# Optimization experiments

Hardware: AMD Instinct MI355X
Metric: run time of the kernel (lower is better)

## Reference

```python
import jax, jax.numpy as jnp
import numpy as np

B, G, N = 32, 512, 512          # batch, group (POMO rollouts), problem size
EMB, H, DK = 128, 8, 16          # embedding_dim, head_num, qkv_dim (H*DK == EMB)
E, FH, K = 8, 512, 2             # num_experts, ff_hidden_dim, top-k
SQRT_EMB = 11.313708498984761    # sqrt(128), model_params['sqrt_embedding_dim']
CLIP = 10.0                      # logit_clipping


def setup_inputs() -> dict:
    key = jax.random.key(0)
    ks = jax.random.split(key, 22)
    s = 0.05
    d = {}
    d["pref"] = jax.random.uniform(ks[0], (2,), dtype=jnp.float32)
    d["graph"] = jax.random.normal(ks[1], (B, 1, EMB), dtype=jnp.float32)
    d["capacity"] = jax.random.uniform(ks[2], (B, G), dtype=jnp.float32)
    d["encoded_nodes"] = jax.random.normal(ks[3], (B, N, EMB), dtype=jnp.float32)
    d["ninf_mask"] = jnp.zeros((B, G, N), dtype=jnp.float32)
    # hyper-network MLP (note: original has NO activations between hyper_fc layers)
    d["fc1_w"] = jax.random.normal(ks[4], (256, 2)) * s
    d["fc1_b"] = jax.random.normal(ks[5], (256,)) * s
    d["fc2_w"] = jax.random.normal(ks[6], (256, 256)) * s
    d["fc2_b"] = jax.random.normal(ks[7], (256,)) * s
    d["fc3_w"] = jax.random.normal(ks[8], (8, 256)) * s
    d["fc3_b"] = jax.random.normal(ks[9], (8,)) * s
    # hyper heads producing the attention weight matrices (Linear(embd_dim=2, out), no bias)
    d["hWq"] = jax.random.normal(ks[10], ((1 + EMB) * H * DK, 2)) * 0.02
    d["hWk"] = jax.random.normal(ks[11], (EMB * H * DK, 2)) * 0.02
    d["hWv"] = jax.random.normal(ks[12], (EMB * H * DK, 2)) * 0.02
    d["hWc"] = jax.random.normal(ks[13], (EMB * H * DK, 2)) * 0.02
    # MoE combine layer: gating (token input + 8-dim pref embedding) and E expert MLPs
    d["gate_w"] = jax.random.normal(ks[14], (H * DK, E)) * s
    d["gate_pref_w"] = jax.random.normal(ks[15], (8, E)) * s
    d["e_w1"] = jax.random.normal(ks[16], (E, FH, H * DK)) * (1.0 / np.sqrt(H * DK))
    d["e_b1"] = jnp.zeros((E, FH), dtype=jnp.float32)
    d["e_w2"] = jax.random.normal(ks[17], (E, EMB, FH)) * (1.0 / np.sqrt(FH))
    d["e_b2"] = jnp.zeros((E, EMB), dtype=jnp.float32)
    d = {k2: v.astype(jnp.float32) for k2, v in d.items()}
    return d


def _heads(x):  # [B, n, H*DK] -> [B, H, n, DK]
    b, n, _ = x.shape
    return x.reshape(b, n, H, DK).transpose(0, 2, 1, 3)


def reference(pref, graph, capacity, encoded_nodes, ninf_mask,
              fc1_w, fc1_b, fc2_w, fc2_b, fc3_w, fc3_b,
              hWq, hWk, hWv, hWc,
              gate_w, gate_pref_w, e_w1, e_b1, e_w2, e_b2):
    # ---- assign(pref): hypernet generates attention weight matrices ----
    h = fc1_w @ pref + fc1_b
    h = fc2_w @ h + fc2_b
    mid = fc3_w @ h + fc3_b                      # [8] == mid_embd_pref
    Wq = (hWq @ mid[0:2]).reshape(H * DK, 1 + EMB)
    Wk = (hWk @ mid[2:4]).reshape(H * DK, EMB)
    Wv = (hWv @ mid[4:6]).reshape(H * DK, EMB)
    Wc = (hWc @ mid[6:8]).reshape(H * DK, EMB)
    # ---- set_kv ----
    k = _heads(encoded_nodes @ Wk.T)             # [B,H,N,DK]
    v = _heads(encoded_nodes @ Wv.T)
    # ---- forward ----
    inp = jnp.concatenate(
        [jnp.broadcast_to(graph, (B, G, EMB)), capacity[:, :, None]], axis=2)
    q = _heads(inp @ Wq.T)                       # [B,H,G,DK]
    score = jnp.einsum('bhgd,bhnd->bhgn', q, k) / jnp.sqrt(jnp.float32(DK))
    score = score + ninf_mask[:, None, :, :]
    attn = jax.nn.softmax(score, axis=3)
    out = jnp.einsum('bhgn,bhnd->bhgd', attn, v)
    out = out.transpose(0, 2, 1, 3).reshape(B, G, H * DK)   # [B,G,128]
    # ---- MoE combine (noisy top-k gating, deterministic at inference) ----
    logits = out @ gate_w + mid @ gate_pref_w    # [B,G,E]
    vals, idx = jax.lax.top_k(logits, K)
    gv = jax.nn.softmax(vals, axis=-1)           # softmax over selected k (T=1)
    gates = jnp.sum(jax.nn.one_hot(idx, E, dtype=out.dtype) * gv[..., None], axis=-2)
    hdn = jax.nn.relu(jnp.einsum('bgi,ehi->bgeh', out, e_w1) + e_b1)
    y = jnp.einsum('bgeh,eoh->bgeo', hdn, e_w2) + e_b2
    moe_out = jnp.einsum('bgeo,bge->bgo', y, gates)          # [B,G,EMB]
    # ---- combine + tanh-clipped masked softmax over nodes ----
    mh = moe_out @ Wc.T                           # [B,G,EMB]
    sc = jnp.einsum('bge,bne->bgn', mh, encoded_nodes) / SQRT_EMB
    probs = jax.nn.softmax(CLIP * jnp.tanh(sc) + ninf_mask, axis=2)
    return probs
```

## Files before the change

kernel.cpp:

```cpp
#include <hip/hip_runtime.h>


typedef __attribute__((ext_vector_type(8))) __bf16 bf16x8;
typedef __attribute__((ext_vector_type(4))) float f32x4;

static constexpr long OFF_MID   = 0;
static constexpr long OFF_PREFL = 8;
static constexpr long OFF_WL    = 16;
static constexpr long OFF_WKB   = 256;
static constexpr long OFF_WVB   = 8448;
static constexpr long OFF_WCB   = 16640;
static constexpr long OFF_QB    = 24832;
static constexpr long OFF_MFLAG = 28928;
static constexpr long OFF_CNT   = 33024;
static constexpr long OFF_TOK   = 33032;
static constexpr long OFF_WGT   = 164104;
static constexpr long OFF_AO    = 295176;
static constexpr long OFF_Y0    = 1343752;
static constexpr long OFF_Y1    = 2392328;
static constexpr long OFF_ENCB  = 3440904;

__device__ __forceinline__ unsigned f2bf(float x) {
  union { float f; unsigned u; } v; v.f = x;
  return ((v.u + 0x7FFFu + ((v.u >> 16) & 1u)) >> 16) & 0xFFFFu;
}
__device__ __forceinline__ float bflo(unsigned u) {
  union { unsigned u; float f; } v; v.u = u << 16; return v.f;
}
__device__ __forceinline__ float bfhi(unsigned u) {
  union { unsigned u; float f; } v; v.u = u & 0xFFFF0000u; return v.f;
}

__global__ __launch_bounds__(256)
void k_prep1(const float* __restrict__ pref, const float* __restrict__ fc1w,
             const float* __restrict__ fc1b, const float* __restrict__ fc2w,
             const float* __restrict__ fc2b, const float* __restrict__ fc3w,
             const float* __restrict__ fc3b, const float* __restrict__ gpw,
             const float* __restrict__ hWq, const float* __restrict__ mask,
             const float* __restrict__ ew1, const float* __restrict__ ew2,
             const float* __restrict__ enc,
             unsigned short* __restrict__ w1b, unsigned short* __restrict__ w2b,
             unsigned short* __restrict__ encb, float* __restrict__ ws) {
  const int bid = blockIdx.x;
  const int tid = threadIdx.x;
  if (bid == 0) {
    __shared__ float h1[256];
    __shared__ float h2[256];
    __shared__ float mid[8];
    const float p0 = pref[0], p1 = pref[1];
    h1[tid] = fc1w[2*tid]*p0 + fc1w[2*tid+1]*p1 + fc1b[tid];
    __syncthreads();
    float s = 0.f;
    for (int j = 0; j < 256; ++j) s = fmaf(fc2w[tid*256+j], h1[j], s);
    h2[tid] = s + fc2b[tid];
    __syncthreads();
    if (tid < 8) {
      float s2 = 0.f;
      for (int j = 0; j < 256; ++j) s2 = fmaf(fc3w[tid*256+j], h2[j], s2);
      mid[tid] = s2 + fc3b[tid];
    }
    __syncthreads();
    if (tid < 8) {
      ws[OFF_MID + tid] = mid[tid];
      float s3 = 0.f;
      for (int i = 0; i < 8; ++i) s3 = fmaf(mid[i], gpw[i*8 + tid], s3);
      ws[OFF_PREFL + tid] = s3;
      ((int*)(ws + OFF_CNT))[tid] = 0;
    }
    if (tid >= 16 && tid < 144) {
      const int o = tid - 16;
      ws[OFF_WL + o] = hWq[((long)o*129 + 128)*2]*mid[0]
                     + hWq[((long)o*129 + 128)*2 + 1]*mid[1];
    }
    return;
  }
  if (bid <= 3072) {
    const int i = (bid-1)*256 + tid;
    const float* src;
    unsigned short* dst;
    if (i < 131072)      { src = ew1 + (long)i*4;          dst = w1b + (long)i*4; }
    else if (i < 262144) { src = ew2 + (long)(i-131072)*4; dst = w2b + (long)(i-131072)*4; }
    else                 { src = enc + (long)(i-262144)*4; dst = encb + (long)(i-262144)*4; }
    const float4 v = *(const float4*)src;
    uint2 p;
    p.x = f2bf(v.x) | (f2bf(v.y) << 16);
    p.y = f2bf(v.z) | (f2bf(v.w) << 16);
    *(uint2*)dst = p;
    return;
  }
  __shared__ int fl[8];
  const int rowbase = (bid - 3073) * 8;
  const int r = tid >> 5, seg = tid & 31;
  if (tid < 8) fl[tid] = 0;
  __syncthreads();
  const float* mrow = mask + (long)(rowbase + r)*512 + seg*16;
  int nz = 0;
#pragma unroll
  for (int c = 0; c < 4; ++c) {
    const float4 v = *(const float4*)(mrow + c*4);
    nz |= (v.x != 0.f) | (v.y != 0.f) | (v.z != 0.f) | (v.w != 0.f);
  }
  if (nz) atomicOr(&fl[r], 1);
  __syncthreads();
  if (tid < 8) ((char*)(ws + OFF_MFLAG))[rowbase + tid] = (char)fl[tid];
}

__global__ __launch_bounds__(256)
void k_prep2(const float* __restrict__ graph,
             const float* __restrict__ hWq, const float* __restrict__ hWk,
             const float* __restrict__ hWv, const float* __restrict__ hWc,
             float* __restrict__ ws) {
  const int bid = blockIdx.x;
  const int tid = threadIdx.x;
  __shared__ float mid[8];
  __shared__ float g[2][128];
  if (tid < 8) mid[tid] = ws[OFF_MID + tid];
  __syncthreads();
  if (bid < 192) {
    const int i = bid*256 + tid;
    if (i < 16384) {
      ((unsigned short*)(ws + OFF_WKB))[i] =
          (unsigned short)f2bf(hWk[2*i]*mid[2] + hWk[2*i+1]*mid[3]);
    } else if (i < 32768) {
      const int j = i - 16384;
      ((unsigned short*)(ws + OFF_WVB))[j] =
          (unsigned short)f2bf(hWv[2*j]*mid[4] + hWv[2*j+1]*mid[5]);
    } else {
      const int j = i - 32768;
      ((unsigned short*)(ws + OFF_WCB))[j] =
          (unsigned short)f2bf(hWc[2*j]*mid[6] + hWc[2*j+1]*mid[7]);
    }
    return;
  }
  const int qb = bid - 192;
  const int b0 = qb*2;
  {
    const int bb = tid >> 7, ii = tid & 127;
    g[bb][ii] = graph[(b0+bb)*128 + ii];
  }
  __syncthreads();
  const float m0 = mid[0], m1 = mid[1];
  const int bb = tid >> 7, o = tid & 127;
  const float* hq = hWq + (long)o*129*2;
  float acc = 0.f;
  for (int i2 = 0; i2 < 128; ++i2) {
    const float w = hq[2*i2]*m0 + hq[2*i2+1]*m1;
    acc = fmaf(g[bb][i2], w, acc);
  }
  ws[OFF_QB + (b0+bb)*128 + o] = acc;
}

__device__ __forceinline__ bf16x8 ld_frag(const unsigned short* base, int row, int bytecol) {
  const int addr = row*256 + (bytecol ^ ((row & 7) << 4));
  return *(const bf16x8*)((const char*)base + addr);
}

__global__ __launch_bounds__(256)
void k_kv(const unsigned short* __restrict__ encb,
          const unsigned short* __restrict__ wkb,
          const unsigned short* __restrict__ wvb,
          unsigned short* __restrict__ Kb, unsigned short* __restrict__ Vtg) {
  __shared__ unsigned short Ws[128*128];
  __shared__ unsigned short Xs[64*128];
  const int tid = threadIdx.x;
  const int nbase = blockIdx.x * 64;
  const unsigned short* Wb = blockIdx.y ? wvb : wkb;
#pragma unroll
  for (int s = 0; s < 8; ++s) {
    const int id = tid + s*256;
    const int fr = id >> 4, c16 = id & 15;
    const uint4 v = *(const uint4*)(Wb + (long)fr*128 + c16*8);
    *(uint4*)((char*)Ws + fr*256 + ((c16*16) ^ ((fr & 7) << 4))) = v;
  }
#pragma unroll
  for (int s = 0; s < 4; ++s) {
    const int id = tid + s*256;
    const int r = id >> 4, c16 = id & 15;
    const uint4 v = *(const uint4*)(encb + (long)(nbase + r)*128 + c16*8);
    *(uint4*)((char*)Xs + r*256 + ((c16*16) ^ ((r & 7) << 4))) = v;
  }
  __syncthreads();
  const int w = tid >> 6, l = tid & 63, lq = l >> 4, lr = l & 15;
  f32x4 acc[2][4];
#pragma unroll
  for (int a = 0; a < 2; ++a)
#pragma unroll
    for (int m = 0; m < 4; ++m) acc[a][m] = (f32x4){0.f, 0.f, 0.f, 0.f};
#pragma unroll
  for (int ks = 0; ks < 4; ++ks) {
    const int bcol = ks*64 + lq*16;
    const bf16x8 a0 = ld_frag(Ws, (2*w  )*16 + lr, bcol);
    const bf16x8 a1 = ld_frag(Ws, (2*w+1)*16 + lr, bcol);
    const bf16x8 b0 = ld_frag(Xs, 0*16 + lr, bcol);
    const bf16x8 b1 = ld_frag(Xs, 1*16 + lr, bcol);
    const bf16x8 b2 = ld_frag(Xs, 2*16 + lr, bcol);
    const bf16x8 b3 = ld_frag(Xs, 3*16 + lr, bcol);
    acc[0][0] = __builtin_amdgcn_mfma_f32_16x16x32_bf16(a0, b0, acc[0][0], 0, 0, 0);
    acc[0][1] = __builtin_amdgcn_mfma_f32_16x16x32_bf16(a0, b1, acc[0][1], 0, 0, 0);
    acc[0][2] = __builtin_amdgcn_mfma_f32_16x16x32_bf16(a0, b2, acc[0][2], 0, 0, 0);
    acc[0][3] = __builtin_amdgcn_mfma_f32_16x16x32_bf16(a0, b3, acc[0][3], 0, 0, 0);
    acc[1][0] = __builtin_amdgcn_mfma_f32_16x16x32_bf16(a1, b0, acc[1][0], 0, 0, 0);
    acc[1][1] = __builtin_amdgcn_mfma_f32_16x16x32_bf16(a1, b1, acc[1][1], 0, 0, 0);
    acc[1][2] = __builtin_amdgcn_mfma_f32_16x16x32_bf16(a1, b2, acc[1][2], 0, 0, 0);
    acc[1][3] = __builtin_amdgcn_mfma_f32_16x16x32_bf16(a1, b3, acc[1][3], 0, 0, 0);
  }
  if (blockIdx.y == 0) {
#pragma unroll
    for (int obi = 0; obi < 2; ++obi) {
      const int o0 = (2*w + obi)*16 + lq*4;
#pragma unroll
      for (int mb = 0; mb < 4; ++mb) {
        const long n = nbase + mb*16 + lr;
        uint2 pp;
        pp.x = f2bf(acc[obi][mb][0]) | (f2bf(acc[obi][mb][1]) << 16);
        pp.y = f2bf(acc[obi][mb][2]) | (f2bf(acc[obi][mb][3]) << 16);
        *(uint2*)(Kb + n*128 + o0) = pp;
      }
    }
  } else {
    const int b = nbase >> 9;
    const int nn0 = nbase & 511;
#pragma unroll
    for (int obi = 0; obi < 2; ++obi) {
      const int o0 = (2*w + obi)*16 + lq*4;
#pragma unroll
      for (int mb = 0; mb < 4; ++mb) {
        const int nn = nn0 + mb*16 + lr;
#pragma unroll
        for (int j = 0; j < 4; ++j) {
          const int o = o0 + j;
          Vtg[(((long)b*8 + (o >> 4))*16 + (o & 15))*512 + nn] =
              (unsigned short)f2bf(acc[obi][mb][j]);
        }
      }
    }
  }
}

__global__ __launch_bounds__(512, 8)
void k_attn(const unsigned short* __restrict__ Kb,
            const unsigned short* __restrict__ Vtg,
            const float* __restrict__ ws, const float* __restrict__ cap,
            const float* __restrict__ mask, unsigned short* __restrict__ AOb) {
  const int bid = blockIdx.x;
  const int b = bid & 31, h = (bid >> 5) & 7, qh = bid >> 8;
  __shared__ unsigned short Kbf[512*24];
  __shared__ unsigned short Vt[16*536];
  __shared__ unsigned short Ps[8*16*40];
  const int tid = threadIdx.x;
#pragma unroll
  for (int it = 0; it < 2; ++it) {
    const int i = tid + it*512;
    const int n = i >> 1, hf = i & 1;
    const uint4 kv = *(const uint4*)(Kb + (long)(b*512 + n)*128 + h*16 + hf*8);
    *(uint4*)(Kbf + n*24 + hf*8) = kv;
    const int d = i >> 6, c = i & 63;
    const uint4 vv = *(const uint4*)(Vtg + ((long)(b*8 + h)*16 + d)*512 + c*8);
    *(uint4*)(Vt + d*536 + c*8) = vv;
  }
  const int w = tid >> 6, l = tid & 63;
  const int lq = l >> 4, lr = l & 15;
  const int grow = qh*128 + w*16 + lr;
  bf16x8 qf;
  {
    union { uint4 u; bf16x8 v; } cv;
    cv.u = make_uint4(0u, 0u, 0u, 0u);
    if (lq < 2) {
      const float* qbp = ws + OFF_QB + b*128 + h*16 + lq*8;
      const float* wlp = ws + OFF_WL + h*16 + lq*8;
      const float cp = cap[b*512 + grow];
      float qv[8];
#pragma unroll
      for (int j = 0; j < 8; ++j) qv[j] = (qbp[j] + cp*wlp[j]) * 0.25f;
      cv.u.x = f2bf(qv[0]) | (f2bf(qv[1]) << 16);
      cv.u.y = f2bf(qv[2]) | (f2bf(qv[3]) << 16);
      cv.u.z = f2bf(qv[4]) | (f2bf(qv[5]) << 16);
      cv.u.w = f2bf(qv[6]) | (f2bf(qv[7]) << 16);
    }
    qf = cv.v;
  }
  const int mf = ((const char*)(ws + OFF_MFLAG))[b*512 + grow];
  const bool usemask = __any(mf != 0);
  unsigned short* Pw = Ps + w*16*40;
  const int psw = (lr & 3) << 3;
  __syncthreads();
  float lsum = 0.f;
  f32x4 oaccA = {0.f, 0.f, 0.f, 0.f};
  f32x4 oaccB = {0.f, 0.f, 0.f, 0.f};
  const float* mrow = mask + ((long)(b*512 + grow))*512 + lq*4;
#pragma unroll 2
  for (int qc = 0; qc < 16; ++qc) {
    const int n0 = qc*32;
    f32x4 s[2];
#pragma unroll
    for (int nb = 0; nb < 2; ++nb) {
      bf16x8 kf;
      {
        union { uint4 u; bf16x8 v; } cv;
        cv.u = make_uint4(0u, 0u, 0u, 0u);
        if (lq < 2) cv.u = *(const uint4*)(Kbf + (n0 + nb*16 + lr)*24 + lq*8);
        kf = cv.v;
      }
      s[nb] = __builtin_amdgcn_mfma_f32_16x16x32_bf16(
          kf, qf, (f32x4){0.f, 0.f, 0.f, 0.f}, 0, 0, 0);
      if (usemask) {
        const float4 mk = *(const float4*)(mrow + n0 + nb*16);
        s[nb][0] += mk.x; s[nb][1] += mk.y; s[nb][2] += mk.z; s[nb][3] += mk.w;
      }
    }
#pragma unroll
    for (int nb = 0; nb < 2; ++nb) {
      const float e0 = __expf(s[nb][0]);
      const float e1 = __expf(s[nb][1]);
      const float e2 = __expf(s[nb][2]);
      const float e3 = __expf(s[nb][3]);
      lsum += (e0 + e1) + (e2 + e3);
      uint2 pp;
      asm("v_cvt_pk_bf16_f32 %0, %1, %2" : "=v"(pp.x) : "v"(e0), "v"(e1));
      asm("v_cvt_pk_bf16_f32 %0, %1, %2" : "=v"(pp.y) : "v"(e2), "v"(e3));
      *(uint2*)(Pw + lr*40 + ((nb*16 + lq*4) ^ psw)) = pp;
    }
    const bf16x8 va = *(const bf16x8*)(Vt + lr*536 + n0 + lq*8);
    const bf16x8 pb = *(const bf16x8*)(Pw + lr*40 + (lq*8 ^ psw));
    if (qc & 1) oaccB = __builtin_amdgcn_mfma_f32_16x16x32_bf16(va, pb, oaccB, 0, 0, 0);
    else        oaccA = __builtin_amdgcn_mfma_f32_16x16x32_bf16(va, pb, oaccA, 0, 0, 0);
  }
  lsum += __shfl_xor(lsum, 16);
  lsum += __shfl_xor(lsum, 32);
  const float inv = 1.f / lsum;
  uint2 op;
  op.x = f2bf((oaccA[0]+oaccB[0])*inv) | (f2bf((oaccA[1]+oaccB[1])*inv) << 16);
  op.y = f2bf((oaccA[2]+oaccB[2])*inv) | (f2bf((oaccA[3]+oaccB[3])*inv) << 16);
  *(uint2*)(AOb + (long)(b*512 + grow)*128 + h*16 + lq*4) = op;
}

__global__ __launch_bounds__(256)
void k_gate(const unsigned short* __restrict__ AOb, const float* __restrict__ gw,
            float* __restrict__ ws) {
  const int tid = threadIdx.x;
  const int t = blockIdx.x*256 + tid;
  const unsigned short* x = AOb + (long)t*128;
  float lg[8];
  {
    const float* pl = ws + OFF_PREFL;
#pragma unroll
    for (int e = 0; e < 8; ++e) lg[e] = pl[e];
  }
  for (int i = 0; i < 128; i += 8) {
    const uint4 xv = *(const uint4*)(x + i);
    float xf[8];
    xf[0] = bflo(xv.x); xf[1] = bfhi(xv.x);
    xf[2] = bflo(xv.y); xf[3] = bfhi(xv.y);
    xf[4] = bflo(xv.z); xf[5] = bfhi(xv.z);
    xf[6] = bflo(xv.w); xf[7] = bfhi(xv.w);
#pragma unroll
    for (int u = 0; u < 8; ++u) {
      const float xi = xf[u];
      const float4 ga = *(const float4*)(gw + (i+u)*8);
      const float4 gb = *(const float4*)(gw + (i+u)*8 + 4);
      lg[0] = fmaf(xi, ga.x, lg[0]); lg[1] = fmaf(xi, ga.y, lg[1]);
      lg[2] = fmaf(xi, ga.z, lg[2]); lg[3] = fmaf(xi, ga.w, lg[3]);
      lg[4] = fmaf(xi, gb.x, lg[4]); lg[5] = fmaf(xi, gb.y, lg[5]);
      lg[6] = fmaf(xi, gb.z, lg[6]); lg[7] = fmaf(xi, gb.w, lg[7]);
    }
  }
  int i0 = 0; float v0 = lg[0];
#pragma unroll
  for (int e = 1; e < 8; ++e) if (lg[e] > v0) { v0 = lg[e]; i0 = e; }
  int i1 = -1; float v1 = -1e30f;
#pragma unroll
  for (int e = 0; e < 8; ++e) if (e != i0 && lg[e] > v1) { v1 = lg[e]; i1 = e; }
  const float e1 = __expf(v1 - v0);
  const float w0 = 1.f / (1.f + e1);
  const float w1 = 1.f - w0;
  __shared__ int bcnt[8];
  __shared__ int gbase[8];
  if (tid < 8) bcnt[tid] = 0;
  __syncthreads();
  const int p0 = atomicAdd(&bcnt[i0], 1);
  const int p1 = atomicAdd(&bcnt[i1], 1);
  __syncthreads();
  if (tid < 8) {
    int* cnt = (int*)(ws + OFF_CNT);
    gbase[tid] = (bcnt[tid] > 0) ? atomicAdd(&cnt[tid], bcnt[tid]) : 0;
  }
  __syncthreads();
  int* tokp = (int*)(ws + OFF_TOK);
  float* wgtp = ws + OFF_WGT;
  const int s0 = gbase[i0] + p0;
  tokp[i0*16384 + s0] = t;
  wgtp[i0*16384 + s0] = w0;
  const int s1 = gbase[i1] + p1;
  tokp[i1*16384 + s1] = t | (1 << 30);
  wgtp[i1*16384 + s1] = w1;
}

__global__ __launch_bounds__(256)
void k_moe(const unsigned short* __restrict__ AOb,
           const unsigned short* __restrict__ w1b,
           const unsigned short* __restrict__ w2b,
           const float* __restrict__ eb1, const float* __restrict__ eb2,
           float* __restrict__ ws,
           unsigned short* __restrict__ Y0b, unsigned short* __restrict__ Y1b) {
  const int e = blockIdx.y;
  const int ce = ((const int*)(ws + OFF_CNT))[e];
  const int base = blockIdx.x * 64;
  if (base >= ce) return;
  const int nt = min(64, ce - base);

  __shared__ unsigned short Xs[64*128];
  __shared__ unsigned short Wts[128*128];
  __shared__ unsigned short Hs[64*128];
  __shared__ float seb1[512];
  __shared__ float seb2[128];
  __shared__ int   stok[64];
  __shared__ float swgt[64];

  const int tid = threadIdx.x;
  if (tid < 64) {
    if (tid < nt) {
      stok[tid] = ((const int*)(ws + OFF_TOK))[e*16384 + base + tid];
      swgt[tid] = (ws + OFF_WGT)[e*16384 + base + tid];
    } else { stok[tid] = -1; swgt[tid] = 0.f; }
  }
  for (int i = tid; i < 512; i += 256) seb1[i] = eb1[e*512 + i];
  if (tid < 128) seb2[tid] = eb2[e*128 + tid];
  __syncthreads();

#pragma unroll
  for (int r4 = 0; r4 < 4; ++r4) {
    const int id = tid + r4*256;
    const int r = id >> 4, c16 = id & 15;
    const int pk = stok[r];
    uint4 v = make_uint4(0u, 0u, 0u, 0u);
    if (pk >= 0) v = *(const uint4*)(AOb + (long)(pk & 0x3FFFFFFF)*128 + c16*8);
    *(uint4*)((char*)Xs + r*256 + ((c16*16) ^ ((r & 7) << 4))) = v;
  }

  const int w  = tid >> 6;
  const int l  = tid & 63;
  const int lq = l >> 4;
  const int lr = l & 15;

  f32x4 yacc[2][4];
#pragma unroll
  for (int a = 0; a < 2; ++a)
#pragma unroll
    for (int m = 0; m < 4; ++m) yacc[a][m] = (f32x4){0.f, 0.f, 0.f, 0.f};

  for (int fc = 0; fc < 4; ++fc) {
    __syncthreads();
    {
      const long wb = (long)(e*512 + fc*128) * 128;
#pragma unroll
      for (int s = 0; s < 8; ++s) {
        const int id = tid + s*256;
        const int fr = id >> 4, c16 = id & 15;
        const uint4 v = *(const uint4*)(w1b + wb + (long)fr*128 + c16*8);
        *(uint4*)((char*)Wts + fr*256 + ((c16*16) ^ ((fr & 7) << 4))) = v;
      }
    }
    __syncthreads();
    f32x4 hacc[2][4];
#pragma unroll
    for (int a = 0; a < 2; ++a)
#pragma unroll
      for (int m = 0; m < 4; ++m) hacc[a][m] = (f32x4){0.f, 0.f, 0.f, 0.f};
#pragma unroll
    for (int ks = 0; ks < 4; ++ks) {
      const int bcol = ks*64 + lq*16;
      const bf16x8 a0 = ld_frag(Wts, (2*w  )*16 + lr, bcol);
      const bf16x8 a1 = ld_frag(Wts, (2*w+1)*16 + lr, bcol);
      const bf16x8 b0 = ld_frag(Xs,  0*16 + lr, bcol);
      const bf16x8 b1 = ld_frag(Xs,  1*16 + lr, bcol);
      const bf16x8 b2 = ld_frag(Xs,  2*16 + lr, bcol);
      const bf16x8 b3 = ld_frag(Xs,  3*16 + lr, bcol);
      hacc[0][0] = __builtin_amdgcn_mfma_f32_16x16x32_bf16(a0, b0, hacc[0][0], 0, 0, 0);
      hacc[0][1] = __builtin_amdgcn_mfma_f32_16x16x32_bf16(a0, b1, hacc[0][1], 0, 0, 0);
      hacc[0][2] = __builtin_amdgcn_mfma_f32_16x16x32_bf16(a0, b2, hacc[0][2], 0, 0, 0);
      hacc[0][3] = __builtin_amdgcn_mfma_f32_16x16x32_bf16(a0, b3, hacc[0][3], 0, 0, 0);
      hacc[1][0] = __builtin_amdgcn_mfma_f32_16x16x32_bf16(a1, b0, hacc[1][0], 0, 0, 0);
      hacc[1][1] = __builtin_amdgcn_mfma_f32_16x16x32_bf16(a1, b1, hacc[1][1], 0, 0, 0);
      hacc[1][2] = __builtin_amdgcn_mfma_f32_16x16x32_bf16(a1, b2, hacc[1][2], 0, 0, 0);
      hacc[1][3] = __builtin_amdgcn_mfma_f32_16x16x32_bf16(a1, b3, hacc[1][3], 0, 0, 0);
    }
    __syncthreads();
#pragma unroll
    for (int fbi = 0; fbi < 2; ++fbi) {
      const int fb = (2*w + fbi)*16 + lq*4;
      const float4 bia = *(const float4*)&seb1[fc*128 + fb];
#pragma unroll
      for (int mb = 0; mb < 4; ++mb) {
        const int m = mb*16 + lr;
        const float h0 = fmaxf(hacc[fbi][mb][0] + bia.x, 0.f);
        const float h1 = fmaxf(hacc[fbi][mb][1] + bia.y, 0.f);
        const float h2 = fmaxf(hacc[fbi][mb][2] + bia.z, 0.f);
        const float h3 = fmaxf(hacc[fbi][mb][3] + bia.w, 0.f);
        uint2 p;
        p.x = f2bf(h0) | (f2bf(h1) << 16);
        p.y = f2bf(h2) | (f2bf(h3) << 16);
        const int bc = (fb*2) ^ ((m & 7) << 4);
        *(uint2*)((char*)Hs + m*256 + bc) = p;
      }
    }
    {
      const long wb = (long)(e*128) * 512 + fc*128;
#pragma unroll
      for (int s = 0; s < 8; ++s) {
        const int id = tid + s*256;
        const int orr = id >> 4, c16 = id & 15;
        const uint4 v = *(const uint4*)(w2b + wb + (long)orr*512 + c16*8);
        *(uint4*)((char*)Wts + orr*256 + ((c16*16) ^ ((orr & 7) << 4))) = v;
      }
    }
    __syncthreads();
#pragma unroll
    for (int ks = 0; ks < 4; ++ks) {
      const int bcol = ks*64 + lq*16;
      const bf16x8 a0 = ld_frag(Wts, (2*w  )*16 + lr, bcol);
      const bf16x8 a1 = ld_frag(Wts, (2*w+1)*16 + lr, bcol);
      const bf16x8 b0 = ld_frag(Hs,  0*16 + lr, bcol);
      const bf16x8 b1 = ld_frag(Hs,  1*16 + lr, bcol);
      const bf16x8 b2 = ld_frag(Hs,  2*16 + lr, bcol);
      const bf16x8 b3 = ld_frag(Hs,  3*16 + lr, bcol);
      yacc[0][0] = __builtin_amdgcn_mfma_f32_16x16x32_bf16(a0, b0, yacc[0][0], 0, 0, 0);
      yacc[0][1] = __builtin_amdgcn_mfma_f32_16x16x32_bf16(a0, b1, yacc[0][1], 0, 0, 0);
      yacc[0][2] = __builtin_amdgcn_mfma_f32_16x16x32_bf16(a0, b2, yacc[0][2], 0, 0, 0);
      yacc[0][3] = __builtin_amdgcn_mfma_f32_16x16x32_bf16(a0, b3, yacc[0][3], 0, 0, 0);
      yacc[1][0] = __builtin_amdgcn_mfma_f32_16x16x32_bf16(a1, b0, yacc[1][0], 0, 0, 0);
      yacc[1][1] = __builtin_amdgcn_mfma_f32_16x16x32_bf16(a1, b1, yacc[1][1], 0, 0, 0);
      yacc[1][2] = __builtin_amdgcn_mfma_f32_16x16x32_bf16(a1, b2, yacc[1][2], 0, 0, 0);
      yacc[1][3] = __builtin_amdgcn_mfma_f32_16x16x32_bf16(a1, b3, yacc[1][3], 0, 0, 0);
    }
  }
#pragma unroll
  for (int obi = 0; obi < 2; ++obi) {
    const int ob = (2*w + obi)*16 + lq*4;
    const float4 b2 = *(const float4*)&seb2[ob];
#pragma unroll
    for (int mb = 0; mb < 4; ++mb) {
      const int tl = mb*16 + lr;
      if (tl < nt) {
        const int pk = stok[tl];
        const int tk = pk & 0x3FFFFFFF;
        const float wgt = swgt[tl];
        unsigned short* Yp = ((pk >> 30) ? Y1b : Y0b) + (long)tk*128 + ob;
        uint2 p;
        p.x = f2bf((yacc[obi][mb][0] + b2.x) * wgt)
            | (f2bf((yacc[obi][mb][1] + b2.y) * wgt) << 16);
        p.y = f2bf((yacc[obi][mb][2] + b2.z) * wgt)
            | (f2bf((yacc[obi][mb][3] + b2.w) * wgt) << 16);
        *(uint2*)Yp = p;
      }
    }
  }
}

__global__ __launch_bounds__(512)
void k_gemm2f(const unsigned short* __restrict__ Y0b,
              const unsigned short* __restrict__ Y1b,
              const unsigned short* __restrict__ wcb,
              const unsigned short* __restrict__ encb,
              const float* __restrict__ mask,
              const char* __restrict__ mflag,
              float* __restrict__ out) {
  const int bid = blockIdx.x;
  const int b = bid & 31, rt = bid >> 5;
  __shared__ unsigned short Amh[64*128];
  __shared__ unsigned short Bch[512*32];
  __shared__ float red[64][9];
  __shared__ char sfl[64];
  const int tid = threadIdx.x;
  const int w = tid >> 6, l = tid & 63, lq = l >> 4, lr = l & 15;
  const long rowbase = (long)b*512 + rt*64;
#pragma unroll
  for (int s = 0; s < 2; ++s) {
    const int id = tid + s*512;
    const int r = id >> 4, c16 = id & 15;
    const long yb = (rowbase + r)*128 + c16*8;
    const uint4 a = *(const uint4*)(Y0b + yb);
    const uint4 c = *(const uint4*)(Y1b + yb);
    uint4 p;
    p.x = f2bf(bflo(a.x)+bflo(c.x)) | (f2bf(bfhi(a.x)+bfhi(c.x)) << 16);
    p.y = f2bf(bflo(a.y)+bflo(c.y)) | (f2bf(bfhi(a.y)+bfhi(c.y)) << 16);
    p.z = f2bf(bflo(a.z)+bflo(c.z)) | (f2bf(bfhi(a.z)+bfhi(c.z)) << 16);
    p.w = f2bf(bflo(a.w)+bflo(c.w)) | (f2bf(bfhi(a.w)+bfhi(c.w)) << 16);
    *(uint4*)((char*)Amh + r*256 + ((c16*16) ^ ((r & 7) << 4))) = p;
  }
#pragma unroll
  for (int s = 0; s < 4; ++s) {
    const int id = tid + s*512;
    const int fr = id >> 4, c16 = id & 15;
    const uint4 v = *(const uint4*)(wcb + (long)fr*128 + c16*8);
    *(uint4*)((char*)Bch + fr*256 + ((c16*16) ^ ((fr & 7) << 4))) = v;
  }
  if (tid < 64) sfl[tid] = mflag[rowbase + tid];
  __syncthreads();
  {
    f32x4 macc[4];
#pragma unroll
    for (int m = 0; m < 4; ++m) macc[m] = (f32x4){0.f, 0.f, 0.f, 0.f};
#pragma unroll
    for (int ks = 0; ks < 4; ++ks) {
      const int bcol = ks*64 + lq*16;
      const bf16x8 a0 = ld_frag(Bch, w*16 + lr, bcol);
      const bf16x8 b0 = ld_frag(Amh, 0*16 + lr, bcol);
      const bf16x8 b1 = ld_frag(Amh, 1*16 + lr, bcol);
      const bf16x8 b2 = ld_frag(Amh, 2*16 + lr, bcol);
      const bf16x8 b3 = ld_frag(Amh, 3*16 + lr, bcol);
      macc[0] = __builtin_amdgcn_mfma_f32_16x16x32_bf16(a0, b0, macc[0], 0, 0, 0);
      macc[1] = __builtin_amdgcn_mfma_f32_16x16x32_bf16(a0, b1, macc[1], 0, 0, 0);
      macc[2] = __builtin_amdgcn_mfma_f32_16x16x32_bf16(a0, b2, macc[2], 0, 0, 0);
      macc[3] = __builtin_amdgcn_mfma_f32_16x16x32_bf16(a0, b3, macc[3], 0, 0, 0);
    }
    __syncthreads();
    const int o0 = w*16 + lq*4;
#pragma unroll
    for (int mb = 0; mb < 4; ++mb) {
      const int m = mb*16 + lr;
      uint2 p;
      p.x = f2bf(macc[mb][0]) | (f2bf(macc[mb][1]) << 16);
      p.y = f2bf(macc[mb][2]) | (f2bf(macc[mb][3]) << 16);
      *(uint2*)((char*)Amh + m*256 + ((o0*2) ^ ((m & 7) << 4))) = p;
    }
  }
  f32x4 acc[4][4];
#pragma unroll
  for (int mi = 0; mi < 4; ++mi)
#pragma unroll
    for (int ni = 0; ni < 4; ++ni) acc[mi][ni] = (f32x4){0.f, 0.f, 0.f, 0.f};
  for (int kc = 0; kc < 4; ++kc) {
    __syncthreads();
#pragma unroll
    for (int s = 0; s < 4; ++s) {
      const int id = tid + s*512;
      const int n = id >> 2, sl = id & 3;
      const uint4 v = *(const uint4*)(encb + ((long)b*512 + n)*128 + kc*32 + sl*8);
      *(uint4*)((char*)Bch + n*64 + ((sl*16) ^ ((n & 3) << 4))) = v;
    }
    __syncthreads();
    bf16x8 af[4], bfr[4];
#pragma unroll
    for (int mi = 0; mi < 4; ++mi) {
      const int r = mi*16 + lr;
      af[mi] = *(const bf16x8*)((const char*)Amh + r*256 + ((kc*64 + lq*16) ^ ((r & 7) << 4)));
    }
#pragma unroll
    for (int ni = 0; ni < 4; ++ni) {
      const int n = w*64 + ni*16 + lr;
      bfr[ni] = *(const bf16x8*)((const char*)Bch + n*64 + ((lq*16) ^ ((n & 3) << 4)));
    }
#pragma unroll
    for (int mi = 0; mi < 4; ++mi)
#pragma unroll
      for (int ni = 0; ni < 4; ++ni)
        acc[mi][ni] = __builtin_amdgcn_mfma_f32_16x16x32_bf16(af[mi], bfr[ni], acc[mi][ni], 0, 0, 0);
  }
  const float ISC = 1.f/11.313708498984761f;
  float rsum[4][4];
#pragma unroll
  for (int mi = 0; mi < 4; ++mi)
#pragma unroll
    for (int j = 0; j < 4; ++j) rsum[mi][j] = 0.f;
#pragma unroll
  for (int mi = 0; mi < 4; ++mi) {
#pragma unroll
    for (int j = 0; j < 4; ++j) {
      const int rl = mi*16 + lq*4 + j;
      const bool um = sfl[rl] != 0;
      const float* mrow = mask + (rowbase + rl)*512 + w*64 + lr;
#pragma unroll
      for (int ni = 0; ni < 4; ++ni) {
        const float sc = acc[mi][ni][j] * ISC;
        const float t = __expf(-2.f * fabsf(sc));
        const float th = (1.f - t) * __builtin_amdgcn_rcpf(1.f + t);
        const float mv = um ? mrow[ni*16] : 0.f;
        const float li = copysignf(th, sc)*10.f + mv;
        const float e = __expf(li - 10.f);
        acc[mi][ni][j] = e;
        rsum[mi][j] += e;
      }
    }
  }
#pragma unroll
  for (int mi = 0; mi < 4; ++mi)
#pragma unroll
    for (int j = 0; j < 4; ++j) {
#pragma unroll
      for (int o = 1; o < 16; o <<= 1) rsum[mi][j] += __shfl_xor(rsum[mi][j], o);
    }
  if (lr == 0) {
#pragma unroll
    for (int mi = 0; mi < 4; ++mi)
#pragma unroll
      for (int j = 0; j < 4; ++j) red[mi*16 + lq*4 + j][w] = rsum[mi][j];
  }
  __syncthreads();
  if (tid < 64) {
    float s = 0.f;
#pragma unroll
    for (int wv = 0; wv < 8; ++wv) s += red[tid][wv];
    red[tid][8] = 1.f / s;
  }
  __syncthreads();
#pragma unroll
  for (int mi = 0; mi < 4; ++mi) {
#pragma unroll
    for (int j = 0; j < 4; ++j) {
      const int rl = mi*16 + lq*4 + j;
      const float inv = red[rl][8];
      float* orow = out + (rowbase + rl)*512 + w*64 + lr;
#pragma unroll
      for (int ni = 0; ni < 4; ++ni) orow[ni*16] = acc[mi][ni][j] * inv;
    }
  }
}

extern "C" void kernel_launch(void* const* d_in, const int* in_sizes, int n_in,
                              void* d_out, int out_size, void* d_ws, size_t ws_size,
                              hipStream_t stream) {
  (void)in_sizes; (void)n_in; (void)out_size; (void)ws_size;
  const float* pref  = (const float*)d_in[0];
  const float* graph = (const float*)d_in[1];
  const float* cap   = (const float*)d_in[2];
  const float* enc   = (const float*)d_in[3];
  const float* mask  = (const float*)d_in[4];
  const float* fc1w  = (const float*)d_in[5];
  const float* fc1b  = (const float*)d_in[6];
  const float* fc2w  = (const float*)d_in[7];
  const float* fc2b  = (const float*)d_in[8];
  const float* fc3w  = (const float*)d_in[9];
  const float* fc3b  = (const float*)d_in[10];
  const float* hWq   = (const float*)d_in[11];
  const float* hWk   = (const float*)d_in[12];
  const float* hWv   = (const float*)d_in[13];
  const float* hWc   = (const float*)d_in[14];
  const float* gw    = (const float*)d_in[15];
  const float* gpw   = (const float*)d_in[16];
  const float* ew1   = (const float*)d_in[17];
  const float* eb1   = (const float*)d_in[18];
  const float* ew2   = (const float*)d_in[19];
  const float* eb2   = (const float*)d_in[20];
  float* ws  = (float*)d_ws;
  float* out = (float*)d_out;
  unsigned short* Kbuf = (unsigned short*)out;
  unsigned short* Vtg  = (unsigned short*)(out + 1048576);
  unsigned short* ew1b = (unsigned short*)(out + 4194304);
  unsigned short* ew2b = (unsigned short*)(out + 4456448);
  unsigned short* AOb  = (unsigned short*)(ws + OFF_AO);
  unsigned short* Y0b  = (unsigned short*)(ws + OFF_Y0);
  unsigned short* Y1b  = (unsigned short*)(ws + OFF_Y1);
  unsigned short* encb = (unsigned short*)(ws + OFF_ENCB);
  unsigned short* wkb  = (unsigned short*)(ws + OFF_WKB);
  unsigned short* wvb  = (unsigned short*)(ws + OFF_WVB);
  unsigned short* wcb  = (unsigned short*)(ws + OFF_WCB);
  const char* mflag = (const char*)(ws + OFF_MFLAG);

  k_prep1<<<5121, 256, 0, stream>>>(pref, fc1w, fc1b, fc2w, fc2b, fc3w, fc3b,
                                    gpw, hWq, mask, ew1, ew2, enc,
                                    ew1b, ew2b, encb, ws);
  k_prep2<<<208, 256, 0, stream>>>(graph, hWq, hWk, hWv, hWc, ws);
  k_kv<<<dim3(256, 2), 256, 0, stream>>>(encb, wkb, wvb, Kbuf, Vtg);
  k_attn<<<1024, 512, 0, stream>>>(Kbuf, Vtg, ws, cap, mask, AOb);
  k_gate<<<64, 256, 0, stream>>>(AOb, gw, ws);
  k_moe<<<dim3(256, 8), 256, 0, stream>>>(AOb, ew1b, ew2b, eb1, eb2, ws, Y0b, Y1b);
  k_gemm2f<<<256, 512, 0, stream>>>(Y0b, Y1b, wcb, encb, mask, mflag, out);
}
```

Measured before the change: 110.2 us.

## Factor attention scores as rank-1 affine in capacity to drop QK MFMA

The query for each group row is qb + cap*wl, so each score q·k can be written as A[n] + cap*B[n], with A and B precomputed once per block from K. The per-tile QK MFMA and the K shared-memory tile are replaced by two per-node float arrays in LDS, and each score becomes one FMA. This removes matrix work and LDS traffic from the inner loop. The scores are now computed in fp32 from fp32 q parts instead of from a bf16-rounded q, which changes rounding slightly.

New measurement: 111.6 us. About the same (+1.3%).

```diff
diff --git a/kernel.cpp b/kernel.cpp
--- a/kernel.cpp
+++ b/kernel.cpp
@@ -244,41 +244,43 @@
             const float* __restrict__ mask, unsigned short* __restrict__ AOb) {
   const int bid = blockIdx.x;
   const int b = bid & 31, h = (bid >> 5) & 7, qh = bid >> 8;
-  __shared__ unsigned short Kbf[512*24];
   __shared__ unsigned short Vt[16*536];
   __shared__ unsigned short Ps[8*16*40];
+  __shared__ float Al[512];
+  __shared__ float Bl[512];
   const int tid = threadIdx.x;
 #pragma unroll
   for (int it = 0; it < 2; ++it) {
     const int i = tid + it*512;
-    const int n = i >> 1, hf = i & 1;
-    const uint4 kv = *(const uint4*)(Kb + (long)(b*512 + n)*128 + h*16 + hf*8);
-    *(uint4*)(Kbf + n*24 + hf*8) = kv;
     const int d = i >> 6, c = i & 63;
     const uint4 vv = *(const uint4*)(Vtg + ((long)(b*8 + h)*16 + d)*512 + c*8);
     *(uint4*)(Vt + d*536 + c*8) = vv;
   }
+  {
+    const int n = tid;
+    const unsigned short* kp = Kb + (long)(b*512 + n)*128 + h*16;
+    const uint4 k0 = *(const uint4*)kp;
+    const uint4 k1 = *(const uint4*)(kp + 8);
+    float kd[16];
+    kd[0]=bflo(k0.x);  kd[1]=bfhi(k0.x);  kd[2]=bflo(k0.y);  kd[3]=bfhi(k0.y);
+    kd[4]=bflo(k0.z);  kd[5]=bfhi(k0.z);  kd[6]=bflo(k0.w);  kd[7]=bfhi(k0.w);
+    kd[8]=bflo(k1.x);  kd[9]=bfhi(k1.x);  kd[10]=bflo(k1.y); kd[11]=bfhi(k1.y);
+    kd[12]=bflo(k1.z); kd[13]=bfhi(k1.z); kd[14]=bflo(k1.w); kd[15]=bfhi(k1.w);
+    const float* qbp = ws + OFF_QB + b*128 + h*16;
+    const float* wlp = ws + OFF_WL + h*16;
+    float dq = 0.f, dw = 0.f;
+#pragma unroll
+    for (int j = 0; j < 16; ++j) {
+      dq = fmaf(qbp[j], kd[j], dq);
+      dw = fmaf(wlp[j], kd[j], dw);
+    }
+    Al[n] = dq * 0.25f;
+    Bl[n] = dw * 0.25f;
+  }
   const int w = tid >> 6, l = tid & 63;
   const int lq = l >> 4, lr = l & 15;
   const int grow = qh*128 + w*16 + lr;
-  bf16x8 qf;
-  {
-    union { uint4 u; bf16x8 v; } cv;
-    cv.u = make_uint4(0u, 0u, 0u, 0u);
-    if (lq < 2) {
-      const float* qbp = ws + OFF_QB + b*128 + h*16 + lq*8;
-      const float* wlp = ws + OFF_WL + h*16 + lq*8;
-      const float cp = cap[b*512 + grow];
-      float qv[8];
-#pragma unroll
-      for (int j = 0; j < 8; ++j) qv[j] = (qbp[j] + cp*wlp[j]) * 0.25f;
-      cv.u.x = f2bf(qv[0]) | (f2bf(qv[1]) << 16);
-      cv.u.y = f2bf(qv[2]) | (f2bf(qv[3]) << 16);
-      cv.u.z = f2bf(qv[4]) | (f2bf(qv[5]) << 16);
-      cv.u.w = f2bf(qv[6]) | (f2bf(qv[7]) << 16);
-    }
-    qf = cv.v;
-  }
+  const float cp = cap[b*512 + grow];
   const int mf = ((const char*)(ws + OFF_MFLAG))[b*512 + grow];
   const bool usemask = __any(mf != 0);
   unsigned short* Pw = Ps + w*16*40;
@@ -291,29 +293,23 @@
 #pragma unroll 2
   for (int qc = 0; qc < 16; ++qc) {
     const int n0 = qc*32;
-    f32x4 s[2];
 #pragma unroll
     for (int nb = 0; nb < 2; ++nb) {
-      bf16x8 kf;
-      {
-        union { uint4 u; bf16x8 v; } cv;
-        cv.u = make_uint4(0u, 0u, 0u, 0u);
-        if (lq < 2) cv.u = *(const uint4*)(Kbf + (n0 + nb*16 + lr)*24 + lq*8);
-        kf = cv.v;
-      }
-      s[nb] = __builtin_amdgcn_mfma_f32_16x16x32_bf16(
-          kf, qf, (f32x4){0.f, 0.f, 0.f, 0.f}, 0, 0, 0);
+      const int nn = n0 + nb*16 + lq*4;
+      const float4 av  = *(const float4*)&Al[nn];
+      const float4 bv4 = *(const float4*)&Bl[nn];
+      float s0 = fmaf(cp, bv4.x, av.x);
+      float s1 = fmaf(cp, bv4.y, av.y);
+      float s2 = fmaf(cp, bv4.z, av.z);
+      float s3 = fmaf(cp, bv4.w, av.w);
       if (usemask) {
         const float4 mk = *(const float4*)(mrow + n0 + nb*16);
-        s[nb][0] += mk.x; s[nb][1] += mk.y; s[nb][2] += mk.z; s[nb][3] += mk.w;
+        s0 += mk.x; s1 += mk.y; s2 += mk.z; s3 += mk.w;
       }
-    }
-#pragma unroll
-    for (int nb = 0; nb < 2; ++nb) {
-      const float e0 = __expf(s[nb][0]);
-      const float e1 = __expf(s[nb][1]);
-      const float e2 = __expf(s[nb][2]);
-      const float e3 = __expf(s[nb][3]);
+      const float e0 = __expf(s0);
+      const float e1 = __expf(s1);
+      const float e2 = __expf(s2);
+      const float e3 = __expf(s3);
       lsum += (e0 + e1) + (e2 + e3);
       uint2 pp;
       asm("v_cvt_pk_bf16_f32 %0, %1, %2" : "=v"(pp.x) : "v"(e0), "v"(e1));
```
